# Kernel optimization log

Measured on AMD Instinct MI355X. Metric: run time of the kernel, lower is better.

## Reference

```python
import jax, jax.numpy as jnp
import numpy as np

DEPTH = 10
N_FEATURES = 1024
N_INTERNAL = 2 ** DEPTH - 1  # 1023
N_LEAVES = 2 ** DEPTH        # 1024
BATCH = 16384


def setup_inputs() -> dict:
    key = jax.random.key(0)
    k_x, k_w, k_b, k_leaf = jax.random.split(key, 4)
    x = jax.random.normal(k_x, (BATCH, N_FEATURES), dtype=jnp.float32)
    # stacked nn.Linear(n_features, 1) weights for all internal nodes
    bound = 1.0 / np.sqrt(N_FEATURES)
    W = jax.random.uniform(k_w, (N_INTERNAL, N_FEATURES), dtype=jnp.float32, minval=-bound, maxval=bound)
    b = jax.random.uniform(k_b, (N_INTERNAL,), dtype=jnp.float32, minval=-bound, maxval=bound)
    leaf_values = jax.random.normal(k_leaf, (N_LEAVES, 1), dtype=jnp.float32) * 0.01
    return {"x": x, "W": W, "b": b, "leaf_values": leaf_values}


def reference(x, W, b, leaf_values):
    # all node gates in one GEMM: [B, n_internal]
    gates = jax.nn.sigmoid(x @ W.T + b)
    # leaf path bits, MSB-first (matches path[::-1] in the original).
    # NOTE: original code increments node_index 0..depth-1 for every leaf
    # (it does NOT do binary-tree child indexing) -- replicated faithfully.
    leaf_ids = jnp.arange(N_LEAVES)
    shifts = DEPTH - 1 - jnp.arange(DEPTH)
    bits = ((leaf_ids[:, None] >> shifts[None, :]) & 1).astype(bool)  # [L, D]
    prob = jnp.ones((x.shape[0], N_LEAVES), dtype=x.dtype)  # [B, L]
    for d in range(DEPTH):  # small fixed loop over tree depth
        p = gates[:, d:d + 1]  # [B, 1]
        prob = prob * jnp.where(bits[:, d][None, :], p, 1.0 - p)
    return prob @ leaf_values  # [B, 1]
```

## Files before the change

### kernel.cpp

```cpp
#include <hip/hip_runtime.h>

#define BATCH    16384
#define NF       1024
#define NWAVES1  2048
#define NWAVES2  4096


template <int CTRL>
__device__ __forceinline__ float dpp_add(float x) {
    int xi = __builtin_bit_cast(int, x);
    int yi = __builtin_amdgcn_update_dpp(xi, xi, CTRL, 0xf, 0xf, false);
    return x + __builtin_bit_cast(float, yi);
}

__device__ __forceinline__ float group16_reduce(float x) {
    x = dpp_add<0xB1>(x);
    x = dpp_add<0x4E>(x);
    x = dpp_add<0x124>(x);
    x = dpp_add<0x128>(x);
    return x;
}

__device__ __forceinline__ float wave_sum(float x) {
    float r = group16_reduce(x);
    int ri = __builtin_bit_cast(int, r);
    float s0 = __builtin_bit_cast(float, __builtin_amdgcn_readlane(ri, 0));
    float s1 = __builtin_bit_cast(float, __builtin_amdgcn_readlane(ri, 16));
    float s2 = __builtin_bit_cast(float, __builtin_amdgcn_readlane(ri, 32));
    float s3 = __builtin_bit_cast(float, __builtin_amdgcn_readlane(ri, 48));
    return (s0 + s1) + (s2 + s3);
}

__global__ __launch_bounds__(256, 2)
void sdt_logits(const float* __restrict__ x,
                const float* __restrict__ W,
                const float* __restrict__ b,
                float* __restrict__ part)
{
    const int lane = threadIdx.x & 63;
    const int wid  = (int)((blockIdx.x * blockDim.x + threadIdx.x) >> 6);

    float4 Wr[10][4];
#pragma unroll
    for (int d = 0; d < 10; ++d)
#pragma unroll
        for (int k = 0; k < 4; ++k)
            Wr[d][k] = *reinterpret_cast<const float4*>(W + d * NF + k * 256 + 4 * lane);
#pragma unroll
    for (int d = 0; d < 10; ++d)
#pragma unroll
        for (int k = 0; k < 4; ++k)
            asm volatile("" : "+v"(Wr[d][k].x), "+v"(Wr[d][k].y),
                              "+v"(Wr[d][k].z), "+v"(Wr[d][k].w));

    float bq[10];
#pragma unroll
    for (int d = 0; d < 10; ++d) bq[d] = b[d] * 0.25f;

    auto load_row = [&](float4 (&dst)[4], int r) {
        const float* xr = x + (size_t)r * NF;
#pragma unroll
        for (int k = 0; k < 4; ++k)
            dst[k] = *reinterpret_cast<const float4*>(xr + k * 256 + 4 * lane);
    };

    auto process_row = [&](const float4 (&xv)[4], int row) {
        float acc[10];
#pragma unroll
        for (int d = 0; d < 10; ++d) {
            float a = 0.0f;
#pragma unroll
            for (int k = 0; k < 4; ++k) {
                a = fmaf(xv[k].x, Wr[d][k].x, a);
                a = fmaf(xv[k].y, Wr[d][k].y, a);
                a = fmaf(xv[k].z, Wr[d][k].z, a);
                a = fmaf(xv[k].w, Wr[d][k].w, a);
            }
            acc[d] = a;
        }
        float* pr = part + (size_t)row * 40 + (lane >> 4);
        const bool st = (lane & 15) == 0;
#pragma unroll
        for (int d = 0; d < 10; ++d) {
            float r = group16_reduce(acc[d]) + bq[d];
            if (st) pr[d * 4] = r;
        }
    };

    float4 xb0[4], xb1[4], xb2[4];
    load_row(xb0, wid);
    load_row(xb1, wid + 1 * NWAVES1);

    load_row(xb2, wid + 2 * NWAVES1); process_row(xb0, wid);
    load_row(xb0, wid + 3 * NWAVES1); process_row(xb1, wid + 1 * NWAVES1);
    load_row(xb1, wid + 4 * NWAVES1); process_row(xb2, wid + 2 * NWAVES1);
    load_row(xb2, wid + 5 * NWAVES1); process_row(xb0, wid + 3 * NWAVES1);
    load_row(xb0, wid + 6 * NWAVES1); process_row(xb1, wid + 4 * NWAVES1);
    load_row(xb1, wid + 7 * NWAVES1); process_row(xb2, wid + 5 * NWAVES1);
    process_row(xb0, wid + 6 * NWAVES1);
    process_row(xb1, wid + 7 * NWAVES1);
}

__global__ __launch_bounds__(256, 2)
void sdt_combine(const float* __restrict__ part,
                 const float* __restrict__ leaf,
                 float* __restrict__ out)
{
    const int lane = threadIdx.x & 63;
    const int wid  = (int)((blockIdx.x * blockDim.x + threadIdx.x) >> 6);

    __shared__ float lv_t[1024];
#pragma unroll
    for (int e = 0; e < 4; ++e) {
        int idx = threadIdx.x * 4 + e;
        lv_t[idx] = leaf[(idx & 63) * 16 + (idx >> 6)];
    }
    __syncthreads();

    for (int row = wid; row < BATCH; row += NWAVES2) {
        float p = 0.0f;
        if (lane < 40) p = part[(size_t)row * 40 + lane];
        p = dpp_add<0xB1>(p);
        p = dpp_add<0x4E>(p);

        int pi = __builtin_bit_cast(int, p);
        float g[10];
#pragma unroll
        for (int d = 0; d < 10; ++d) {
            float z = __builtin_bit_cast(float, __builtin_amdgcn_readlane(pi, 4 * d));
            g[d] = __builtin_amdgcn_rcpf(1.0f + __expf(-z));
        }

        float s9[8];
#pragma unroll
        for (int j = 0; j < 8; ++j) {
            float La = lv_t[(2 * j) * 64 + lane];
            float Lb = lv_t[(2 * j + 1) * 64 + lane];
            s9[j] = fmaf(g[9], Lb - La, La);
        }
        float s8[4];
#pragma unroll
        for (int j = 0; j < 4; ++j)
            s8[j] = fmaf(g[8], s9[2 * j + 1] - s9[2 * j], s9[2 * j]);
        float s7[2];
#pragma unroll
        for (int j = 0; j < 2; ++j)
            s7[j] = fmaf(g[7], s8[2 * j + 1] - s8[2 * j], s8[2 * j]);
        float s6 = fmaf(g[6], s7[1] - s7[0], s7[0]);

        float w = 1.0f;
#pragma unroll
        for (int d = 0; d < 6; ++d) {
            int bit = (lane >> (5 - d)) & 1;
            w *= bit ? g[d] : (1.0f - g[d]);
        }

        float v = wave_sum(w * s6);
        if (lane == 0) out[row] = v;
    }
}

extern "C" void kernel_launch(void* const* d_in, const int* in_sizes, int n_in,
                              void* d_out, int out_size, void* d_ws, size_t ws_size,
                              hipStream_t stream) {
    const float* x    = (const float*)d_in[0];
    const float* W    = (const float*)d_in[1];
    const float* b    = (const float*)d_in[2];
    const float* leaf = (const float*)d_in[3];
    float* out  = (float*)d_out;
    float* part = (float*)d_ws;

    sdt_logits<<<512, 256, 0, stream>>>(x, W, b, part);
    sdt_combine<<<1024, 256, 0, stream>>>(part, leaf, out);
}
```

Before: 28.59 us.

## Split each row across four waves by feature quarter and move bias to combine

The logits kernel now gives each wave one 256-feature quarter of a row instead of the whole row. It launches four times as many waves, each holding 10 float4 weight registers instead of 40, so occupancy rises from 2 to 4 blocks per CU. The explicit triple-buffered software pipeline is replaced by a simple loop, and latency hiding now relies on more resident waves. Each wave reduces across the full wavefront with shuffles and writes one partial per depth. The bias add moves into the combine kernel.

```diff
diff --git a/kernel.cpp b/kernel.cpp
--- a/kernel.cpp
+++ b/kernel.cpp
@@ -2,7 +2,7 @@
 
 #define BATCH    16384
 #define NF       1024
-#define NWAVES1  2048
+#define NWAVES1  8192
 #define NWAVES2  4096
 
 
@@ -31,78 +31,50 @@
     return (s0 + s1) + (s2 + s3);
 }
 
-__global__ __launch_bounds__(256, 2)
+__global__ __launch_bounds__(256, 4)
 void sdt_logits(const float* __restrict__ x,
                 const float* __restrict__ W,
-                const float* __restrict__ b,
                 float* __restrict__ part)
 {
     const int lane = threadIdx.x & 63;
-    const int wid  = (int)((blockIdx.x * blockDim.x + threadIdx.x) >> 6);
+    const int wg   = (int)((blockIdx.x * blockDim.x + threadIdx.x) >> 6);
+    const int q    = wg & 3;
+    const int rseq = wg >> 2;
 
-    float4 Wr[10][4];
+    float4 Wr[10];
 #pragma unroll
     for (int d = 0; d < 10; ++d)
-#pragma unroll
-        for (int k = 0; k < 4; ++k)
-            Wr[d][k] = *reinterpret_cast<const float4*>(W + d * NF + k * 256 + 4 * lane);
+        Wr[d] = *reinterpret_cast<const float4*>(W + d * NF + q * 256 + 4 * lane);
 #pragma unroll
     for (int d = 0; d < 10; ++d)
-#pragma unroll
-        for (int k = 0; k < 4; ++k)
-            asm volatile("" : "+v"(Wr[d][k].x), "+v"(Wr[d][k].y),
-                              "+v"(Wr[d][k].z), "+v"(Wr[d][k].w));
+        asm volatile("" : "+v"(Wr[d].x), "+v"(Wr[d].y),
+                          "+v"(Wr[d].z), "+v"(Wr[d].w));
 
-    float bq[10];
-#pragma unroll
-    for (int d = 0; d < 10; ++d) bq[d] = b[d] * 0.25f;
+    const float* xq = x + q * 256 + 4 * lane;
 
-    auto load_row = [&](float4 (&dst)[4], int r) {
-        const float* xr = x + (size_t)r * NF;
-#pragma unroll
-        for (int k = 0; k < 4; ++k)
-            dst[k] = *reinterpret_cast<const float4*>(xr + k * 256 + 4 * lane);
-    };
+    for (int i = 0; i < 8; ++i) {
+        const int row = rseq + i * 2048;
 
-    auto process_row = [&](const float4 (&xv)[4], int row) {
-        float acc[10];
+        const float4 xv = *reinterpret_cast<const float4*>(xq + (size_t)row * NF);
+
+        float* pr = part + (size_t)row * 40 + q;
 #pragma unroll
         for (int d = 0; d < 10; ++d) {
-            float a = 0.0f;
-#pragma unroll
-            for (int k = 0; k < 4; ++k) {
-                a = fmaf(xv[k].x, Wr[d][k].x, a);
-                a = fmaf(xv[k].y, Wr[d][k].y, a);
-                a = fmaf(xv[k].z, Wr[d][k].z, a);
-                a = fmaf(xv[k].w, Wr[d][k].w, a);
-            }
-            acc[d] = a;
+            float a = xv.x * Wr[d].x;
+            a = fmaf(xv.y, Wr[d].y, a);
+            a = fmaf(xv.z, Wr[d].z, a);
+            a = fmaf(xv.w, Wr[d].w, a);
+            float r = group16_reduce(a);
+            r += __shfl_xor(r, 16, 64);
+            r += __shfl_xor(r, 32, 64);
+            if (lane == 0) pr[d * 4] = r;
         }
-        float* pr = part + (size_t)row * 40 + (lane >> 4);
-        const bool st = (lane & 15) == 0;
-#pragma unroll
-        for (int d = 0; d < 10; ++d) {
-            float r = group16_reduce(acc[d]) + bq[d];
-            if (st) pr[d * 4] = r;
-        }
-    };
-
-    float4 xb0[4], xb1[4], xb2[4];
-    load_row(xb0, wid);
-    load_row(xb1, wid + 1 * NWAVES1);
-
-    load_row(xb2, wid + 2 * NWAVES1); process_row(xb0, wid);
-    load_row(xb0, wid + 3 * NWAVES1); process_row(xb1, wid + 1 * NWAVES1);
-    load_row(xb1, wid + 4 * NWAVES1); process_row(xb2, wid + 2 * NWAVES1);
-    load_row(xb2, wid + 5 * NWAVES1); process_row(xb0, wid + 3 * NWAVES1);
-    load_row(xb0, wid + 6 * NWAVES1); process_row(xb1, wid + 4 * NWAVES1);
-    load_row(xb1, wid + 7 * NWAVES1); process_row(xb2, wid + 5 * NWAVES1);
-    process_row(xb0, wid + 6 * NWAVES1);
-    process_row(xb1, wid + 7 * NWAVES1);
+    }
 }
 
 __global__ __launch_bounds__(256, 2)
 void sdt_combine(const float* __restrict__ part,
+                 const float* __restrict__ b,
                  const float* __restrict__ leaf,
                  float* __restrict__ out)
 {
@@ -115,6 +87,11 @@
         int idx = threadIdx.x * 4 + e;
         lv_t[idx] = leaf[(idx & 63) * 16 + (idx >> 6)];
     }
+
+    float bias[10];
+#pragma unroll
+    for (int d = 0; d < 10; ++d) bias[d] = b[d];
+
     __syncthreads();
 
     for (int row = wid; row < BATCH; row += NWAVES2) {
@@ -127,7 +104,8 @@
         float g[10];
 #pragma unroll
         for (int d = 0; d < 10; ++d) {
-            float z = __builtin_bit_cast(float, __builtin_amdgcn_readlane(pi, 4 * d));
+            float z = __builtin_bit_cast(float, __builtin_amdgcn_readlane(pi, 4 * d))
+                      + bias[d];
             g[d] = __builtin_amdgcn_rcpf(1.0f + __expf(-z));
         }
 
@@ -170,6 +148,6 @@
     float* out  = (float*)d_out;
     float* part = (float*)d_ws;
 
-    sdt_logits<<<512, 256, 0, stream>>>(x, W, b, part);
-    sdt_combine<<<1024, 256, 0, stream>>>(part, leaf, out);
+    sdt_logits<<<2048, 256, 0, stream>>>(x, W, part);
+    sdt_combine<<<1024, 256, 0, stream>>>(part, b, leaf, out);
 }
```

New measurement: 37.48 us. 31.1% more time.
